# Performance work log

Hardware: AMD Instinct MI355X
Metric: run time of the kernel (lower is better)

Reference implementation:

```python
import jax, jax.numpy as jnp
import numpy as np
from jax import lax

B, C, IC, H, W = 4, 64, 32, 64, 64


def _conv(x, w, b, stride, pad):
    y = lax.conv_general_dilated(
        x, w, (stride, stride), [(pad, pad), (pad, pad)],
        dimension_numbers=('NCHW', 'OIHW', 'NCHW'))
    return y + b[None, :, None, None]


def setup_inputs() -> dict:
    key = jax.random.key(0)
    ks = jax.random.split(key, 15)
    s = 0.05
    inp = {
        'x': jax.random.normal(ks[0], (B, C, H, W), jnp.float32),
        # GEunit convs (3x3)
        'd1_w': jax.random.normal(ks[1], (C, C, 3, 3), jnp.float32) * s,
        'd1_b': jax.random.normal(ks[2], (C,), jnp.float32) * s,
        'd2_w': jax.random.normal(ks[3], (C, C, 3, 3), jnp.float32) * s,
        'd2_b': jax.random.normal(ks[4], (C,), jnp.float32) * s,
        'd3_w': jax.random.normal(ks[5], (C, C, 3, 3), jnp.float32) * s,
        'd3_b': jax.random.normal(ks[6], (C,), jnp.float32) * s,
        # 1x1 projections
        'g_w': jax.random.normal(ks[7], (IC, C, 1, 1), jnp.float32) * s,
        'g_b': jax.random.normal(ks[8], (IC,), jnp.float32) * s,
        'th_w': jax.random.normal(ks[9], (IC, C, 1, 1), jnp.float32) * s,
        'th_b': jax.random.normal(ks[10], (IC,), jnp.float32) * s,
        'ph_w': jax.random.normal(ks[11], (IC, C, 1, 1), jnp.float32) * s,
        'ph_b': jax.random.normal(ks[12], (IC,), jnp.float32) * s,
        # output projection (zero-init in original; random here for nontrivial baseline)
        'w_w': jax.random.normal(ks[13], (C, IC, 1, 1), jnp.float32) * s,
        'w_b': jax.random.normal(ks[14], (C,), jnp.float32) * s,
    }
    return inp


def _forward(x, d1_w, d1_b, d2_w, d2_b, d3_w, d3_b,
             g_w, g_b, th_w, th_b, ph_w, ph_b, w_w, w_b):
    lrelu = lambda v: jnp.where(v >= 0, v, 0.2 * v)
    y = lrelu(_conv(x, d1_w, d1_b, 2, 1))
    y = lrelu(_conv(y, d2_w, d2_b, 2, 1))
    y = _conv(y, d3_w, d3_b, 2, 1)
    y = jax.image.resize(y, (x.shape[0], x.shape[1], x.shape[2], x.shape[3]),
                         method='bilinear')  # align_corners=False equivalent
    am = jax.nn.sigmoid(y) * x  # attention_map, [B,C,H,W]

    b, c, h, w = am.shape
    n = h * w
    g_x = _conv(am, g_w, g_b, 1, 0).reshape(b, IC, n)      # [B,IC,N]
    theta = _conv(am, th_w, th_b, 1, 0).reshape(b, IC, n)  # [B,IC,N]
    phi = _conv(am, ph_w, ph_b, 1, 0).reshape(b, IC, n)    # [B,IC,N]

    # f[b,i,j] = theta[:, i] . phi[:, j];  softmax over dim=1 (the i axis)
    f = jnp.einsum('bci,bcj->bij', theta, phi)             # [B,N,N]
    f_div_C = jax.nn.softmax(f, axis=1)
    y2 = jnp.einsum('bij,bjc->bic', f_div_C, g_x.transpose(0, 2, 1))  # [B,N,IC]
    y2 = y2.transpose(0, 2, 1).reshape(b, IC, h, w)

    W_y = _conv(y2, w_w, w_b, 1, 0)
    z = W_y + am
    return z * x


def reference(x, d1_w, d1_b, d2_w, d2_b, d3_w, d3_b,
              g_w, g_b, th_w, th_b, ph_w, ph_b, w_w, w_b):
    return _forward(x, d1_w, d1_b, d2_w, d2_b, d3_w, d3_b,
                    g_w, g_b, th_w, th_b, ph_w, ph_b, w_w, w_b)
```

## Files before the change

kernel.cpp:

```cpp
#include <hip/hip_runtime.h>

#define B_ 4
#define C_ 64
#define IC_ 32
#define N_ 4096
#define LOG2E 1.44269504088896341f

typedef __attribute__((ext_vector_type(8))) short short8;
typedef __attribute__((ext_vector_type(4))) float floatx4;
typedef unsigned short ushort_t;

__device__ __forceinline__ unsigned short f2bf(float f) {
  unsigned u = __float_as_uint(f);
  u += 0x7FFFu + ((u >> 16) & 1u);
  return (unsigned short)(u >> 16);
}
__device__ __forceinline__ float bf2f(unsigned short h) {
  return __uint_as_float(((unsigned)h) << 16);
}

__global__ void __launch_bounds__(256) pack_xw_k(
    const float* __restrict__ x, unsigned short* __restrict__ xclp,
    const float* __restrict__ d1_w, const float* __restrict__ d2_w, const float* __restrict__ d3_w,
    const float* __restrict__ th_w, const float* __restrict__ ph_w, const float* __restrict__ g_w,
    const float* __restrict__ th_b, const float* __restrict__ ph_b, const float* __restrict__ g_b,
    unsigned short* __restrict__ wpk, unsigned short* __restrict__ wproj, float* __restrict__ bproj)
{
  __shared__ float s[64][65];
  const int t = threadIdx.x;
  if (blockIdx.x < 256) {
    const int b = blockIdx.x >> 6, h = blockIdx.x & 63;
    for (int idx = t; idx < 4096; idx += 256) {
      int c = idx >> 6, w = idx & 63;
      s[c][w] = x[((size_t)(b * 64 + c)) * 4096 + h * 64 + w];
    }
    __syncthreads();
    for (int idx = t; idx < 4096; idx += 256) {
      int w = idx >> 6, c = idx & 63;
      xclp[(((size_t)b * 66 + h + 1) * 66 + (w + 1)) * 64 + c] = f2bf(s[c][w]);
    }
  } else {
    const int tid = (blockIdx.x - 256) * 256 + t;
    for (int idx = tid; idx < 3 * 36864; idx += 16 * 256) {
      int cv = idx / 36864, r = idx % 36864;
      int tap = r / 4096, r2 = r % 4096;
      int oc = r2 >> 6, ic = r2 & 63;
      const float* src = (cv == 0) ? d1_w : (cv == 1) ? d2_w : d3_w;
      wpk[(size_t)cv * 36864 + tap * 4096 + oc * 64 + ic] = f2bf(src[oc * 576 + ic * 9 + tap]);
    }
    for (int idx = tid; idx < 6144; idx += 16 * 256) {
      int m = idx >> 6, ic = idx & 63;
      float v = (m < 32) ? LOG2E * th_w[m * 64 + ic]
              : (m < 64) ? ph_w[(m - 32) * 64 + ic]
                         : g_w[(m - 64) * 64 + ic];
      wproj[m * 64 + ic] = f2bf(v);
    }
    for (int m = tid; m < 96; m += 16 * 256) {
      bproj[m] = (m < 32) ? LOG2E * th_b[m] : (m < 64) ? ph_b[m - 32] : g_b[m - 64];
    }
  }
}

template<int IN_PW, int OUT_H, bool LRELU, bool OUT_BF16>
__global__ void __launch_bounds__(64) convmf_k(
    const unsigned short* __restrict__ xin, const unsigned short* __restrict__ wp,
    const float* __restrict__ bias, unsigned short* __restrict__ obf,
    float* __restrict__ of32)
{
  constexpr int NTILES = OUT_H * OUT_H / 16;
  const int lane = threadIdx.x;
  const int n15 = lane & 15, quad = lane >> 4;
  int bx = blockIdx.x;
  const int octile = bx & 3; bx >>= 2;
  const int otile = bx % NTILES;
  const int b = bx / NTILES;
  const int o = otile * 16 + n15;
  const int oh = o / OUT_H, ow = o % OUT_H;
  const unsigned short* xb = xin + (size_t)b * IN_PW * IN_PW * 64;
  floatx4 acc = {0.f, 0.f, 0.f, 0.f};
#pragma unroll
  for (int tap = 0; tap < 9; ++tap) {
    const int kh = tap / 3, kw = tap % 3;
    const unsigned short* xpix = xb + ((size_t)(oh * 2 + kh) * IN_PW + (ow * 2 + kw)) * 64;
#pragma unroll
    for (int ks = 0; ks < 2; ++ks) {
      short8 af = *reinterpret_cast<const short8*>(
          wp + ((size_t)tap * 64 + octile * 16 + n15) * 64 + ks * 32 + quad * 8);
      short8 bf = *reinterpret_cast<const short8*>(xpix + ks * 32 + quad * 8);
      acc = __builtin_amdgcn_mfma_f32_16x16x32_bf16(af, bf, acc, 0, 0, 0);
    }
  }
  const float4 bv = *reinterpret_cast<const float4*>(bias + octile * 16 + quad * 4);
  float v[4] = {acc[0] + bv.x, acc[1] + bv.y, acc[2] + bv.z, acc[3] + bv.w};
  if (LRELU) {
#pragma unroll
    for (int r = 0; r < 4; ++r) v[r] = (v[r] >= 0.f) ? v[r] : 0.2f * v[r];
  }
  if (OUT_BF16) {
    constexpr int OPW = OUT_H + 2;
    unsigned short pk[4];
#pragma unroll
    for (int r = 0; r < 4; ++r) pk[r] = f2bf(v[r]);
    *reinterpret_cast<uint2*>(
        obf + (((size_t)b * OPW + oh + 1) * OPW + (ow + 1)) * 64 + octile * 16 + quad * 4) =
        *reinterpret_cast<uint2*>(pk);
  } else {
    *reinterpret_cast<float4*>(
        of32 + ((size_t)b * OUT_H * OUT_H + o) * 64 + octile * 16 + quad * 4) =
        *reinterpret_cast<float4*>(v);
  }
}

__global__ void __launch_bounds__(256) upsproj_k(
    const float* __restrict__ y3cl, const float* __restrict__ x,
    const unsigned short* __restrict__ wproj, const float* __restrict__ bproj,
    unsigned short* __restrict__ am_cl, unsigned short* __restrict__ thph,
    unsigned short* __restrict__ g16)
{
  const int b = blockIdx.x >> 6, oh = blockIdx.x & 63;
  const int t = threadIdx.x;
  __shared__ float s0[512], s1[512];
  __shared__ unsigned short s_am[64][72];
  float sh = (oh + 0.5f) * 0.125f - 0.5f;
  float fh = floorf(sh); float ah = sh - fh; int h0 = (int)fh;
  int h0c = min(7, max(0, h0)), h1c = min(7, max(0, h0 + 1));
  const float* yb = y3cl + (size_t)b * 4096;
  for (int i = t; i < 512; i += 256) { s0[i] = yb[h0c * 512 + i]; s1[i] = yb[h1c * 512 + i]; }
  __syncthreads();
  {
    const int ow = t >> 2, cq = t & 3;
    float sw = (ow + 0.5f) * 0.125f - 0.5f;
    float fw = floorf(sw); float aw = sw - fw; int w0 = (int)fw;
    int w0c = min(7, max(0, w0)), w1c = min(7, max(0, w0 + 1));
    const int n = oh * 64 + ow;
    const float* xb = x + (size_t)b * 64 * 4096 + n;
    unsigned short* ap = am_cl + ((size_t)b * N_ + n) * 64 + cq * 16;
#pragma unroll
    for (int u = 0; u < 4; ++u) {
      int c0 = cq * 16 + u * 4;
      float4 a00 = *reinterpret_cast<const float4*>(&s0[w0c * 64 + c0]);
      float4 a01 = *reinterpret_cast<const float4*>(&s0[w1c * 64 + c0]);
      float4 a10 = *reinterpret_cast<const float4*>(&s1[w0c * 64 + c0]);
      float4 a11 = *reinterpret_cast<const float4*>(&s1[w1c * 64 + c0]);
      float i0[4] = {a00.x * (1.f - aw) + a01.x * aw, a00.y * (1.f - aw) + a01.y * aw,
                     a00.z * (1.f - aw) + a01.z * aw, a00.w * (1.f - aw) + a01.w * aw};
      float i1[4] = {a10.x * (1.f - aw) + a11.x * aw, a10.y * (1.f - aw) + a11.y * aw,
                     a10.z * (1.f - aw) + a11.z * aw, a10.w * (1.f - aw) + a11.w * aw};
      unsigned short pk[4];
#pragma unroll
      for (int vi = 0; vi < 4; ++vi) {
        float vv = i0[vi] * (1.f - ah) + i1[vi] * ah;
        float xv = xb[(size_t)(c0 + vi) * 4096];
        float sig = 1.f / (1.f + __expf(-vv));
        pk[vi] = f2bf(sig * xv);
      }
      uint2 pkt = *reinterpret_cast<uint2*>(pk);
      *reinterpret_cast<uint2*>(ap + u * 4) = pkt;
      *reinterpret_cast<uint2*>(&s_am[ow][c0]) = pkt;
    }
  }
  __syncthreads();
  const int wave = t >> 6, lane = t & 63;
  const int n15 = lane & 15, quad = lane >> 4;
  const int n = oh * 64 + wave * 16 + n15;
  const unsigned short* srow = &s_am[wave * 16 + n15][0];
  const short8 bf0 = *reinterpret_cast<const short8*>(srow + quad * 8);
  const short8 bf1 = *reinterpret_cast<const short8*>(srow + 32 + quad * 8);
#pragma unroll
  for (int mt = 0; mt < 6; ++mt) {
    short8 a0 = *reinterpret_cast<const short8*>(wproj + ((size_t)mt * 16 + n15) * 64 + quad * 8);
    short8 a1 = *reinterpret_cast<const short8*>(wproj + ((size_t)mt * 16 + n15) * 64 + 32 + quad * 8);
    floatx4 acc = {0.f, 0.f, 0.f, 0.f};
    acc = __builtin_amdgcn_mfma_f32_16x16x32_bf16(a0, bf0, acc, 0, 0, 0);
    acc = __builtin_amdgcn_mfma_f32_16x16x32_bf16(a1, bf1, acc, 0, 0, 0);
    const float4 bv = *reinterpret_cast<const float4*>(bproj + mt * 16 + quad * 4);
    float v[4] = {acc[0] + bv.x, acc[1] + bv.y, acc[2] + bv.z, acc[3] + bv.w};
    if (mt < 4) {
      unsigned short pk[4];
#pragma unroll
      for (int r = 0; r < 4; ++r) pk[r] = f2bf(v[r]);
      *reinterpret_cast<uint2*>(thph + ((size_t)b * N_ + n) * 64 + mt * 16 + quad * 4) =
          *reinterpret_cast<uint2*>(pk);
    } else {
#pragma unroll
      for (int r = 0; r < 4; ++r)
        g16[((size_t)b * 32 + (mt - 4) * 16 + quad * 4 + r) * N_ + n] = f2bf(v[r]);
    }
  }
}

__global__ void __launch_bounds__(256) attn_stats_k(
    const unsigned short* __restrict__ thph, float* __restrict__ lpart)
{
  const int b  = blockIdx.y;
  const int iz = blockIdx.z;
  const int t = threadIdx.x, wave = t >> 6, lane = t & 63;
  const int n15 = lane & 15, quad = lane >> 4;
  const int jw = blockIdx.x * 256 + wave * 64;
  const unsigned short* base = thph + (size_t)b * N_ * 64;
  short8 bv[4];
#pragma unroll
  for (int v = 0; v < 4; ++v)
    bv[v] = *reinterpret_cast<const short8*>(base + (size_t)(jw + v * 16 + n15) * 64 + 32 + quad * 8);
  float ls[4] = {0.f, 0.f, 0.f, 0.f};
  const unsigned short* ap = base + (size_t)(iz * 256 + n15) * 64 + quad * 8;
  short8 ac = *reinterpret_cast<const short8*>(ap);
  for (int st = 0; st < 16; ++st) {
    short8 an = *reinterpret_cast<const short8*>(ap + (size_t)((st < 15) ? st + 1 : st) * 1024);
#pragma unroll
    for (int v = 0; v < 4; ++v) {
      floatx4 z = {0.f, 0.f, 0.f, 0.f};
      z = __builtin_amdgcn_mfma_f32_16x16x32_bf16(ac, bv[v], z, 0, 0, 0);
      ls[v] += (__builtin_amdgcn_exp2f(z[0]) + __builtin_amdgcn_exp2f(z[1]))
             + (__builtin_amdgcn_exp2f(z[2]) + __builtin_amdgcn_exp2f(z[3]));
    }
    ac = an;
  }
#pragma unroll
  for (int v = 0; v < 4; ++v) {
    ls[v] += __shfl_xor(ls[v], 16);
    ls[v] += __shfl_xor(ls[v], 32);
  }
  if (quad == 0) {
#pragma unroll
    for (int v = 0; v < 4; ++v)
      lpart[((size_t)iz * B_ + b) * N_ + jw + v * 16 + n15] = ls[v];
  }
}

__global__ void __launch_bounds__(256) scale_g_k(
    const float* __restrict__ lpart, unsigned short* __restrict__ g16)
{
  const int b = blockIdx.y;
  const int c0 = blockIdx.z * 8;
  const int j = blockIdx.x * 256 + threadIdx.x;
  float l = 0.f;
#pragma unroll
  for (int iz = 0; iz < 16; ++iz) l += lpart[((size_t)iz * B_ + b) * N_ + j];
  const float rl = 1.f / l;
  unsigned short* gp = g16 + ((size_t)b * 32 + c0) * N_ + j;
#pragma unroll
  for (int c = 0; c < 8; ++c) {
    gp[(size_t)c * N_] = f2bf(bf2f(gp[(size_t)c * N_]) * rl);
  }
}

#define PHI_PITCH 40
#define G_PITCH   136
__global__ void __launch_bounds__(256, 4) attn_pv_k(
    const unsigned short* __restrict__ thph, const unsigned short* __restrict__ g16,
    unsigned short* __restrict__ y2p)
{
  const int b  = blockIdx.y;
  const int jq = blockIdx.z;
  const int t = threadIdx.x, wave = t >> 6, lane = t & 63;
  const int n15 = lane & 15, quad = lane >> 4;
  const int iw = blockIdx.x * 64 + wave * 16;
  const unsigned short* base = thph + (size_t)b * N_ * 64;
  const unsigned short* gs   = g16  + (size_t)b * 32 * N_;
  __shared__ unsigned short phi_lds[2][128 * PHI_PITCH];
  __shared__ unsigned short g_lds[2][32 * G_PITCH];

  const short8 bth = *reinterpret_cast<const short8*>(base + (size_t)(iw + n15) * 64 + quad * 8);
  floatx4 Y0 = {0.f, 0.f, 0.f, 0.f}, Y1 = {0.f, 0.f, 0.f, 0.f};

  const int rphi = wave * 32 + (lane >> 2), cph = lane & 3;
  const int cg   = wave * 8  + (lane >> 4), chg = lane & 15;

  uint4 sp0, sp1, sg0, sg1;
  const int jbase = jq * 1024;
  sp0 = *reinterpret_cast<const uint4*>(base + (size_t)(jbase + rphi) * 64 + 32 + cph * 8);
  sp1 = *reinterpret_cast<const uint4*>(base + (size_t)(jbase + rphi + 16) * 64 + 32 + cph * 8);
  sg0 = *reinterpret_cast<const uint4*>(gs + (size_t)cg * N_ + jbase + chg * 8);
  sg1 = *reinterpret_cast<const uint4*>(gs + (size_t)(cg + 4) * N_ + jbase + chg * 8);
  *reinterpret_cast<uint4*>(&phi_lds[0][rphi * PHI_PITCH + cph * 8]) = sp0;
  *reinterpret_cast<uint4*>(&phi_lds[0][(rphi + 16) * PHI_PITCH + cph * 8]) = sp1;
  *reinterpret_cast<uint4*>(&g_lds[0][cg * G_PITCH + chg * 8]) = sg0;
  *reinterpret_cast<uint4*>(&g_lds[0][(cg + 4) * G_PITCH + chg * 8]) = sg1;
  __syncthreads();

  int j0 = jbase;
  for (int ch = 0; ch < 8; ++ch, j0 += 128) {
    const int cur = ch & 1;
    if (ch < 7) {
      const int jn = j0 + 128;
      sp0 = *reinterpret_cast<const uint4*>(base + (size_t)(jn + rphi) * 64 + 32 + cph * 8);
      sp1 = *reinterpret_cast<const uint4*>(base + (size_t)(jn + rphi + 16) * 64 + 32 + cph * 8);
      sg0 = *reinterpret_cast<const uint4*>(gs + (size_t)cg * N_ + jn + chg * 8);
      sg1 = *reinterpret_cast<const uint4*>(gs + (size_t)(cg + 4) * N_ + jn + chg * 8);
    }
    const unsigned short* phb = &phi_lds[cur][0];
    const unsigned short* glb = &g_lds[cur][0];
    unsigned pk[8][2];
#pragma unroll
    for (int jt = 0; jt < 8; ++jt) {
      short8 aph = *reinterpret_cast<const short8*>(phb + (jt * 16 + n15) * PHI_PITCH + quad * 8);
      floatx4 z = {0.f, 0.f, 0.f, 0.f};
      z = __builtin_amdgcn_mfma_f32_16x16x32_bf16(aph, bth, z, 0, 0, 0);
      float e0 = __builtin_amdgcn_exp2f(z[0]), e1 = __builtin_amdgcn_exp2f(z[1]);
      float e2 = __builtin_amdgcn_exp2f(z[2]), e3 = __builtin_amdgcn_exp2f(z[3]);
      pk[jt][0] = __builtin_amdgcn_perm(__float_as_uint(e1), __float_as_uint(e0), 0x07060302);
      pk[jt][1] = __builtin_amdgcn_perm(__float_as_uint(e3), __float_as_uint(e2), 0x07060302);
    }
#pragma unroll
    for (int sg = 0; sg < 4; ++sg) {
      union { unsigned u[4]; short8 v; } pa, gb0, gb1;
      pa.u[0] = pk[2 * sg][0];     pa.u[1] = pk[2 * sg][1];
      pa.u[2] = pk[2 * sg + 1][0]; pa.u[3] = pk[2 * sg + 1][1];
      const unsigned short* gr0 = glb + n15 * G_PITCH + sg * 32 + quad * 4;
      const unsigned short* gr1 = glb + (16 + n15) * G_PITCH + sg * 32 + quad * 4;
      uint2 lo0 = *reinterpret_cast<const uint2*>(gr0);
      uint2 hi0 = *reinterpret_cast<const uint2*>(gr0 + 16);
      uint2 lo1 = *reinterpret_cast<const uint2*>(gr1);
      uint2 hi1 = *reinterpret_cast<const uint2*>(gr1 + 16);
      gb0.u[0] = lo0.x; gb0.u[1] = lo0.y; gb0.u[2] = hi0.x; gb0.u[3] = hi0.y;
      gb1.u[0] = lo1.x; gb1.u[1] = lo1.y; gb1.u[2] = hi1.x; gb1.u[3] = hi1.y;
      Y0 = __builtin_amdgcn_mfma_f32_16x16x32_bf16(pa.v, gb0.v, Y0, 0, 0, 0);
      Y1 = __builtin_amdgcn_mfma_f32_16x16x32_bf16(pa.v, gb1.v, Y1, 0, 0, 0);
    }
    if (ch < 7) {
      const int nb = cur ^ 1;
      *reinterpret_cast<uint4*>(&phi_lds[nb][rphi * PHI_PITCH + cph * 8]) = sp0;
      *reinterpret_cast<uint4*>(&phi_lds[nb][(rphi + 16) * PHI_PITCH + cph * 8]) = sp1;
      *reinterpret_cast<uint4*>(&g_lds[nb][cg * G_PITCH + chg * 8]) = sg0;
      *reinterpret_cast<uint4*>(&g_lds[nb][(cg + 4) * G_PITCH + chg * 8]) = sg1;
    }
    __syncthreads();
  }
  unsigned w0[2], w1[2];
  w0[0] = ((unsigned)f2bf(Y0[1]) << 16) | f2bf(Y0[0]);
  w0[1] = ((unsigned)f2bf(Y0[3]) << 16) | f2bf(Y0[2]);
  w1[0] = ((unsigned)f2bf(Y1[1]) << 16) | f2bf(Y1[0]);
  w1[1] = ((unsigned)f2bf(Y1[3]) << 16) | f2bf(Y1[2]);
  *reinterpret_cast<uint2*>(
      y2p + (((size_t)jq * B_ + b) * 32 + n15) * N_ + iw + quad * 4) =
      *reinterpret_cast<uint2*>(w0);
  *reinterpret_cast<uint2*>(
      y2p + (((size_t)jq * B_ + b) * 32 + 16 + n15) * N_ + iw + quad * 4) =
      *reinterpret_cast<uint2*>(w1);
}

__global__ void __launch_bounds__(256) final_k(
    const unsigned short* __restrict__ y2p, const float* __restrict__ w_w,
    const float* __restrict__ w_b, const unsigned short* __restrict__ am_cl,
    const float* __restrict__ x, float* __restrict__ out)
{
  const int n0 = (blockIdx.x * 256 + threadIdx.x) * 2;
  const int o0 = blockIdx.y * 8;
  const int b  = blockIdx.z;
  float a0[8], a1[8];
#pragma unroll
  for (int u = 0; u < 8; ++u) { a0[u] = w_b[o0 + u]; a1[u] = a0[u]; }
  for (int c = 0; c < 32; ++c) {
    float s0 = 0.f, s1 = 0.f;
#pragma unroll
    for (int ph = 0; ph < 4; ++ph) {
      unsigned v = *reinterpret_cast<const unsigned*>(
          y2p + (((size_t)ph * B_ + b) * 32 + c) * N_ + n0);
      s0 += bf2f((unsigned short)(v & 0xffffu));
      s1 += bf2f((unsigned short)(v >> 16));
    }
#pragma unroll
    for (int u = 0; u < 8; ++u) {
      float wv = w_w[(o0 + u) * 32 + c];
      a0[u] += wv * s0; a1[u] += wv * s1;
    }
  }
  const short8 am0 = *reinterpret_cast<const short8*>(am_cl + ((size_t)b * N_ + n0) * 64 + o0);
  const short8 am1 = *reinterpret_cast<const short8*>(am_cl + ((size_t)b * N_ + n0 + 1) * 64 + o0);
#pragma unroll
  for (int u = 0; u < 8; ++u) {
    size_t off = ((size_t)b * 64 + o0 + u) * N_ + n0;
    float2 xv = *reinterpret_cast<const float2*>(x + off);
    float2 ov;
    ov.x = (a0[u] + bf2f((unsigned short)am0[u])) * xv.x;
    ov.y = (a1[u] + bf2f((unsigned short)am1[u])) * xv.y;
    *reinterpret_cast<float2*>(out + off) = ov;
  }
}

extern "C" void kernel_launch(void* const* d_in, const int* in_sizes, int n_in,
                              void* d_out, int out_size, void* d_ws, size_t ws_size,
                              hipStream_t stream) {
  const float* x    = (const float*)d_in[0];
  const float* d1_w = (const float*)d_in[1];
  const float* d1_b = (const float*)d_in[2];
  const float* d2_w = (const float*)d_in[3];
  const float* d2_b = (const float*)d_in[4];
  const float* d3_w = (const float*)d_in[5];
  const float* d3_b = (const float*)d_in[6];
  const float* g_w  = (const float*)d_in[7];
  const float* g_b  = (const float*)d_in[8];
  const float* th_w = (const float*)d_in[9];
  const float* th_b = (const float*)d_in[10];
  const float* ph_w = (const float*)d_in[11];
  const float* ph_b = (const float*)d_in[12];
  const float* w_w  = (const float*)d_in[13];
  const float* w_b  = (const float*)d_in[14];
  float* out = (float*)d_out;

  char* p = (char*)d_ws;
  unsigned short* am_cl = (unsigned short*)p;  p += (size_t)B_ * N_ * 64 * 2;
  unsigned short* thph  = (unsigned short*)p;  p += (size_t)B_ * N_ * 64 * 2;
  unsigned short* g16   = (unsigned short*)p;  p += (size_t)B_ * 32 * N_ * 2;
  float* lpart          = (float*)p;           p += (size_t)16 * B_ * N_ * 4;
  unsigned short* y2p   = (unsigned short*)p;  p += (size_t)4 * B_ * 32 * N_ * 2;
  float* y3cl           = (float*)p;           p += (size_t)B_ * 64 * 64 * 4;
  unsigned short* wpk   = (unsigned short*)p;  p += (size_t)3 * 36864 * 2;
  unsigned short* wproj = (unsigned short*)p;  p += (size_t)96 * 64 * 2;
  float* bproj          = (float*)p;           p += (size_t)96 * 4;
  char* zbase = p;
  unsigned short* xclp  = (unsigned short*)p;  p += (size_t)B_ * 66 * 66 * 64 * 2;
  unsigned short* y1clp = (unsigned short*)p;  p += (size_t)B_ * 34 * 34 * 64 * 2;
  unsigned short* y2clp = (unsigned short*)p;  p += (size_t)B_ * 18 * 18 * 64 * 2;
  const size_t zbytes = (size_t)(p - zbase);

  hipMemsetAsync(zbase, 0, zbytes, stream);
  pack_xw_k<<<272, 256, 0, stream>>>(x, xclp, d1_w, d2_w, d3_w, th_w, ph_w, g_w,
                                     th_b, ph_b, g_b, wpk, wproj, bproj);
  convmf_k<66, 32, true,  true ><<<1024, 64, 0, stream>>>(xclp,  wpk,             d1_b, y1clp, nullptr);
  convmf_k<34, 16, true,  true ><<<256,  64, 0, stream>>>(y1clp, wpk + 36864,     d2_b, y2clp, nullptr);
  convmf_k<18,  8, false, false><<<64,   64, 0, stream>>>(y2clp, wpk + 2 * 36864, d3_b, nullptr, y3cl);
  upsproj_k<<<256, 256, 0, stream>>>(y3cl, x, wproj, bproj, am_cl, thph, g16);
  attn_stats_k<<<dim3(16, 4, 16), 256, 0, stream>>>(thph, lpart);
  scale_g_k<<<dim3(16, 4, 4), 256, 0, stream>>>(lpart, g16);
  attn_pv_k<<<dim3(64, 4, 4), 256, 0, stream>>>(thph, g16, y2p);
  final_k<<<dim3(8, 8, 4), 256, 0, stream>>>(y2p, w_w, w_b, am_cl, x, out);
}
```

Measured before the change: 156.1 us.

## Fuse third conv into upsample kernel and widen attention PV tile per wave

The third stride-2 conv is dropped as a separate launch: each upsproj block now recomputes, with MFMA, the two 8-pixel rows of conv3 output it needs and writes them straight to LDS, which removes one launch and the y3cl round trip. The cost is redundant conv3 work, since many blocks recompute the same rows. Separately, attn_pv_k now has each wave handle 32 query columns instead of 16, so every phi and g tile loaded into LDS is reused twice as often. That halves the grid and lowers the occupancy hint to 2 in exchange for more registers per wave.

```diff
diff --git a/kernel.cpp b/kernel.cpp
--- a/kernel.cpp
+++ b/kernel.cpp
@@ -112,7 +112,8 @@
 }
 
 __global__ void __launch_bounds__(256) upsproj_k(
-    const float* __restrict__ y3cl, const float* __restrict__ x,
+    const unsigned short* __restrict__ y2clp, const unsigned short* __restrict__ wp3,
+    const float* __restrict__ b3, const float* __restrict__ x,
     const unsigned short* __restrict__ wproj, const float* __restrict__ bproj,
     unsigned short* __restrict__ am_cl, unsigned short* __restrict__ thph,
     unsigned short* __restrict__ g16)
@@ -124,8 +125,30 @@
   float sh = (oh + 0.5f) * 0.125f - 0.5f;
   float fh = floorf(sh); float ah = sh - fh; int h0 = (int)fh;
   int h0c = min(7, max(0, h0)), h1c = min(7, max(0, h0 + 1));
-  const float* yb = y3cl + (size_t)b * 4096;
-  for (int i = t; i < 512; i += 256) { s0[i] = yb[h0c * 512 + i]; s1[i] = yb[h1c * 512 + i]; }
+  {
+    const int wave = t >> 6, lane = t & 63;
+    const int n15 = lane & 15, quad = lane >> 4;
+    const int hrow = (n15 < 8) ? h0c : h1c;
+    const int ow8 = n15 & 7;
+    const unsigned short* xb2 = y2clp + (size_t)b * 18 * 18 * 64;
+    floatx4 acc = {0.f, 0.f, 0.f, 0.f};
+#pragma unroll
+    for (int tap = 0; tap < 9; ++tap) {
+      const int kh = tap / 3, kw = tap % 3;
+      const unsigned short* xpix = xb2 + ((size_t)(hrow * 2 + kh) * 18 + (ow8 * 2 + kw)) * 64;
+#pragma unroll
+      for (int ks = 0; ks < 2; ++ks) {
+        short8 af = *reinterpret_cast<const short8*>(
+            wp3 + ((size_t)tap * 64 + wave * 16 + n15) * 64 + ks * 32 + quad * 8);
+        short8 bf = *reinterpret_cast<const short8*>(xpix + ks * 32 + quad * 8);
+        acc = __builtin_amdgcn_mfma_f32_16x16x32_bf16(af, bf, acc, 0, 0, 0);
+      }
+    }
+    const float4 bv = *reinterpret_cast<const float4*>(b3 + wave * 16 + quad * 4);
+    float4 st = {acc[0] + bv.x, acc[1] + bv.y, acc[2] + bv.z, acc[3] + bv.w};
+    float* dst = (n15 < 8) ? s0 : s1;
+    *reinterpret_cast<float4*>(&dst[(size_t)ow8 * 64 + wave * 16 + quad * 4]) = st;
+  }
   __syncthreads();
   {
     const int ow = t >> 2, cq = t & 3;
@@ -247,7 +270,7 @@
 
 #define PHI_PITCH 40
 #define G_PITCH   136
-__global__ void __launch_bounds__(256, 4) attn_pv_k(
+__global__ void __launch_bounds__(256, 2) attn_pv_k(
     const unsigned short* __restrict__ thph, const unsigned short* __restrict__ g16,
     unsigned short* __restrict__ y2p)
 {
@@ -255,14 +278,16 @@
   const int jq = blockIdx.z;
   const int t = threadIdx.x, wave = t >> 6, lane = t & 63;
   const int n15 = lane & 15, quad = lane >> 4;
-  const int iw = blockIdx.x * 64 + wave * 16;
+  const int iw = blockIdx.x * 128 + wave * 32;
   const unsigned short* base = thph + (size_t)b * N_ * 64;
   const unsigned short* gs   = g16  + (size_t)b * 32 * N_;
   __shared__ unsigned short phi_lds[2][128 * PHI_PITCH];
   __shared__ unsigned short g_lds[2][32 * G_PITCH];
 
-  const short8 bth = *reinterpret_cast<const short8*>(base + (size_t)(iw + n15) * 64 + quad * 8);
-  floatx4 Y0 = {0.f, 0.f, 0.f, 0.f}, Y1 = {0.f, 0.f, 0.f, 0.f};
+  const short8 bth0 = *reinterpret_cast<const short8*>(base + (size_t)(iw + n15) * 64 + quad * 8);
+  const short8 bth1 = *reinterpret_cast<const short8*>(base + (size_t)(iw + 16 + n15) * 64 + quad * 8);
+  floatx4 Y00 = {0.f, 0.f, 0.f, 0.f}, Y01 = {0.f, 0.f, 0.f, 0.f};
+  floatx4 Y10 = {0.f, 0.f, 0.f, 0.f}, Y11 = {0.f, 0.f, 0.f, 0.f};
 
   const int rphi = wave * 32 + (lane >> 2), cph = lane & 3;
   const int cg   = wave * 8  + (lane >> 4), chg = lane & 15;
@@ -291,22 +316,28 @@
     }
     const unsigned short* phb = &phi_lds[cur][0];
     const unsigned short* glb = &g_lds[cur][0];
-    unsigned pk[8][2];
-#pragma unroll
-    for (int jt = 0; jt < 8; ++jt) {
-      short8 aph = *reinterpret_cast<const short8*>(phb + (jt * 16 + n15) * PHI_PITCH + quad * 8);
-      floatx4 z = {0.f, 0.f, 0.f, 0.f};
-      z = __builtin_amdgcn_mfma_f32_16x16x32_bf16(aph, bth, z, 0, 0, 0);
-      float e0 = __builtin_amdgcn_exp2f(z[0]), e1 = __builtin_amdgcn_exp2f(z[1]);
-      float e2 = __builtin_amdgcn_exp2f(z[2]), e3 = __builtin_amdgcn_exp2f(z[3]);
-      pk[jt][0] = __builtin_amdgcn_perm(__float_as_uint(e1), __float_as_uint(e0), 0x07060302);
-      pk[jt][1] = __builtin_amdgcn_perm(__float_as_uint(e3), __float_as_uint(e2), 0x07060302);
-    }
 #pragma unroll
     for (int sg = 0; sg < 4; ++sg) {
-      union { unsigned u[4]; short8 v; } pa, gb0, gb1;
-      pa.u[0] = pk[2 * sg][0];     pa.u[1] = pk[2 * sg][1];
-      pa.u[2] = pk[2 * sg + 1][0]; pa.u[3] = pk[2 * sg + 1][1];
+      unsigned pk0[4], pk1[4];
+#pragma unroll
+      for (int jtl = 0; jtl < 2; ++jtl) {
+        const int jt = sg * 2 + jtl;
+        short8 aph = *reinterpret_cast<const short8*>(phb + (jt * 16 + n15) * PHI_PITCH + quad * 8);
+        floatx4 z0 = {0.f, 0.f, 0.f, 0.f}, z1 = {0.f, 0.f, 0.f, 0.f};
+        z0 = __builtin_amdgcn_mfma_f32_16x16x32_bf16(aph, bth0, z0, 0, 0, 0);
+        z1 = __builtin_amdgcn_mfma_f32_16x16x32_bf16(aph, bth1, z1, 0, 0, 0);
+        float a0 = __builtin_amdgcn_exp2f(z0[0]), a1 = __builtin_amdgcn_exp2f(z0[1]);
+        float a2 = __builtin_amdgcn_exp2f(z0[2]), a3 = __builtin_amdgcn_exp2f(z0[3]);
+        float b0f = __builtin_amdgcn_exp2f(z1[0]), b1f = __builtin_amdgcn_exp2f(z1[1]);
+        float b2f = __builtin_amdgcn_exp2f(z1[2]), b3f = __builtin_amdgcn_exp2f(z1[3]);
+        pk0[jtl * 2 + 0] = __builtin_amdgcn_perm(__float_as_uint(a1), __float_as_uint(a0), 0x07060302);
+        pk0[jtl * 2 + 1] = __builtin_amdgcn_perm(__float_as_uint(a3), __float_as_uint(a2), 0x07060302);
+        pk1[jtl * 2 + 0] = __builtin_amdgcn_perm(__float_as_uint(b1f), __float_as_uint(b0f), 0x07060302);
+        pk1[jtl * 2 + 1] = __builtin_amdgcn_perm(__float_as_uint(b3f), __float_as_uint(b2f), 0x07060302);
+      }
+      union { unsigned u[4]; short8 v; } pa0, pa1, gb0, gb1;
+      pa0.u[0] = pk0[0]; pa0.u[1] = pk0[1]; pa0.u[2] = pk0[2]; pa0.u[3] = pk0[3];
+      pa1.u[0] = pk1[0]; pa1.u[1] = pk1[1]; pa1.u[2] = pk1[2]; pa1.u[3] = pk1[3];
       const unsigned short* gr0 = glb + n15 * G_PITCH + sg * 32 + quad * 4;
       const unsigned short* gr1 = glb + (16 + n15) * G_PITCH + sg * 32 + quad * 4;
       uint2 lo0 = *reinterpret_cast<const uint2*>(gr0);
@@ -315,8 +346,10 @@
       uint2 hi1 = *reinterpret_cast<const uint2*>(gr1 + 16);
       gb0.u[0] = lo0.x; gb0.u[1] = lo0.y; gb0.u[2] = hi0.x; gb0.u[3] = hi0.y;
       gb1.u[0] = lo1.x; gb1.u[1] = lo1.y; gb1.u[2] = hi1.x; gb1.u[3] = hi1.y;
-      Y0 = __builtin_amdgcn_mfma_f32_16x16x32_bf16(pa.v, gb0.v, Y0, 0, 0, 0);
-      Y1 = __builtin_amdgcn_mfma_f32_16x16x32_bf16(pa.v, gb1.v, Y1, 0, 0, 0);
+      Y00 = __builtin_amdgcn_mfma_f32_16x16x32_bf16(pa0.v, gb0.v, Y00, 0, 0, 0);
+      Y01 = __builtin_amdgcn_mfma_f32_16x16x32_bf16(pa0.v, gb1.v, Y01, 0, 0, 0);
+      Y10 = __builtin_amdgcn_mfma_f32_16x16x32_bf16(pa1.v, gb0.v, Y10, 0, 0, 0);
+      Y11 = __builtin_amdgcn_mfma_f32_16x16x32_bf16(pa1.v, gb1.v, Y11, 0, 0, 0);
     }
     if (ch < 7) {
       const int nb = cur ^ 1;
@@ -327,17 +360,24 @@
     }
     __syncthreads();
   }
-  unsigned w0[2], w1[2];
-  w0[0] = ((unsigned)f2bf(Y0[1]) << 16) | f2bf(Y0[0]);
-  w0[1] = ((unsigned)f2bf(Y0[3]) << 16) | f2bf(Y0[2]);
-  w1[0] = ((unsigned)f2bf(Y1[1]) << 16) | f2bf(Y1[0]);
-  w1[1] = ((unsigned)f2bf(Y1[3]) << 16) | f2bf(Y1[2]);
-  *reinterpret_cast<uint2*>(
-      y2p + (((size_t)jq * B_ + b) * 32 + n15) * N_ + iw + quad * 4) =
-      *reinterpret_cast<uint2*>(w0);
-  *reinterpret_cast<uint2*>(
-      y2p + (((size_t)jq * B_ + b) * 32 + 16 + n15) * N_ + iw + quad * 4) =
-      *reinterpret_cast<uint2*>(w1);
+  unsigned w00[2], w01[2], w10[2], w11[2];
+  w00[0] = ((unsigned)f2bf(Y00[1]) << 16) | f2bf(Y00[0]);
+  w00[1] = ((unsigned)f2bf(Y00[3]) << 16) | f2bf(Y00[2]);
+  w01[0] = ((unsigned)f2bf(Y01[1]) << 16) | f2bf(Y01[0]);
+  w01[1] = ((unsigned)f2bf(Y01[3]) << 16) | f2bf(Y01[2]);
+  w10[0] = ((unsigned)f2bf(Y10[1]) << 16) | f2bf(Y10[0]);
+  w10[1] = ((unsigned)f2bf(Y10[3]) << 16) | f2bf(Y10[2]);
+  w11[0] = ((unsigned)f2bf(Y11[1]) << 16) | f2bf(Y11[0]);
+  w11[1] = ((unsigned)f2bf(Y11[3]) << 16) | f2bf(Y11[2]);
+  const size_t orow = ((size_t)jq * B_ + b) * 32;
+  *reinterpret_cast<uint2*>(y2p + (orow + n15) * N_ + iw + quad * 4) =
+      *reinterpret_cast<uint2*>(w00);
+  *reinterpret_cast<uint2*>(y2p + (orow + 16 + n15) * N_ + iw + quad * 4) =
+      *reinterpret_cast<uint2*>(w01);
+  *reinterpret_cast<uint2*>(y2p + (orow + n15) * N_ + iw + 16 + quad * 4) =
+      *reinterpret_cast<uint2*>(w10);
+  *reinterpret_cast<uint2*>(y2p + (orow + 16 + n15) * N_ + iw + 16 + quad * 4) =
+      *reinterpret_cast<uint2*>(w11);
 }
 
 __global__ void __launch_bounds__(256) final_k(
@@ -405,7 +445,6 @@
   unsigned short* g16   = (unsigned short*)p;  p += (size_t)B_ * 32 * N_ * 2;
   float* lpart          = (float*)p;           p += (size_t)16 * B_ * N_ * 4;
   unsigned short* y2p   = (unsigned short*)p;  p += (size_t)4 * B_ * 32 * N_ * 2;
-  float* y3cl           = (float*)p;           p += (size_t)B_ * 64 * 64 * 4;
   unsigned short* wpk   = (unsigned short*)p;  p += (size_t)3 * 36864 * 2;
   unsigned short* wproj = (unsigned short*)p;  p += (size_t)96 * 64 * 2;
   float* bproj          = (float*)p;           p += (size_t)96 * 4;
@@ -418,12 +457,12 @@
   hipMemsetAsync(zbase, 0, zbytes, stream);
   pack_xw_k<<<272, 256, 0, stream>>>(x, xclp, d1_w, d2_w, d3_w, th_w, ph_w, g_w,
                                      th_b, ph_b, g_b, wpk, wproj, bproj);
-  convmf_k<66, 32, true,  true ><<<1024, 64, 0, stream>>>(xclp,  wpk,             d1_b, y1clp, nullptr);
-  convmf_k<34, 16, true,  true ><<<256,  64, 0, stream>>>(y1clp, wpk + 36864,     d2_b, y2clp, nullptr);
-  convmf_k<18,  8, false, false><<<64,   64, 0, stream>>>(y2clp, wpk + 2 * 36864, d3_b, nullptr, y3cl);
-  upsproj_k<<<256, 256, 0, stream>>>(y3cl, x, wproj, bproj, am_cl, thph, g16);
+  convmf_k<66, 32, true,  true ><<<1024, 64, 0, stream>>>(xclp,  wpk,         d1_b, y1clp, nullptr);
+  convmf_k<34, 16, true,  true ><<<256,  64, 0, stream>>>(y1clp, wpk + 36864, d2_b, y2clp, nullptr);
+  upsproj_k<<<256, 256, 0, stream>>>(y2clp, wpk + 2 * 36864, d3_b, x, wproj, bproj,
+                                     am_cl, thph, g16);
   attn_stats_k<<<dim3(16, 4, 16), 256, 0, stream>>>(thph, lpart);
   scale_g_k<<<dim3(16, 4, 4), 256, 0, stream>>>(lpart, g16);
-  attn_pv_k<<<dim3(64, 4, 4), 256, 0, stream>>>(thph, g16, y2p);
+  attn_pv_k<<<dim3(32, 4, 4), 256, 0, stream>>>(thph, g16, y2p);
   final_k<<<dim3(8, 8, 4), 256, 0, stream>>>(y2p, w_w, w_b, am_cl, x, out);
 }
```

Result: faster. 151.6 us, median of 2 (-2.9%).
